# Kernel optimization log

Measured on AMD Instinct MI355X. Metric: run time of the kernel, lower is better.

The kernel has to match this reference:

```python
import jax, jax.numpy as jnp
import numpy as np

PARTS = [list(range(0, 17)), list(range(17, 22)), list(range(22, 27)),
         list(range(27, 36)), list(range(36, 42)), list(range(42, 48)),
         list(range(48, 68))]
NUM_PARTS = len(PARTS)
V_JOINTS = max(max(p) for p in PARTS) + 1  # 68
# joint -> part index (same as get_corr_joints)
JOINTS = np.zeros((V_JOINTS,), dtype=np.int32)
for j, part in enumerate(PARTS):
    for i in part:
        JOINTS[i] = j
BN_EPS = 1e-5


def setup_inputs() -> dict:
    key = jax.random.key(0)
    k0, k1, k2 = jax.random.split(key, 3)
    N, C, T, V = 512, 1024, 1, V_JOINTS
    x = jax.random.normal(k0, (N, C, T, V), dtype=jnp.float32)
    conv1_w = jax.random.normal(k1, (C // 4, C), dtype=jnp.float32) * 0.02  # 1x1 conv C->C/4
    conv1_b = jnp.zeros((C // 4,), dtype=jnp.float32)
    conv2_w = jax.random.normal(k2, (2,), dtype=jnp.float32) * 0.5  # 1x1 conv 2->1
    conv2_b = jnp.zeros((), dtype=jnp.float32)
    bn_gamma = jnp.ones((C,), dtype=jnp.float32)
    bn_beta = jnp.zeros((C,), dtype=jnp.float32)
    return {"x": x, "conv1_w": conv1_w, "conv1_b": conv1_b,
            "conv2_w": conv2_w, "conv2_b": conv2_b,
            "bn_gamma": bn_gamma, "bn_beta": bn_beta}


def _forward(x, conv1_w, conv1_b, conv2_w, conv2_b, bn_gamma, bn_beta):
    N, C, T, V = x.shape  # T must be 1 (required by original .view)
    joints = jnp.asarray(JOINTS)
    P = NUM_PARTS
    # part-wise mean pool over joints: (V,P) normalized one-hot
    M = jax.nn.one_hot(joints, P, dtype=x.dtype)
    M = M / jnp.sum(M, axis=0, keepdims=True)
    x_parts = jnp.einsum('nctv,vp->nctp', x, M)            # (N,C,T,P)
    # conv1: 1x1, C -> C/4
    h = jnp.einsum('nctp,oc->notp', x_parts, conv1_w) + conv1_b[None, :, None, None]
    x_cap = jnp.mean(h, axis=1, keepdims=True)             # channel avg pool
    x_cmp = jnp.max(h, axis=1, keepdims=True)              # channel max pool
    # conv2: 1x1, 2 -> 1 (cat order is (avg, max))
    att = conv2_w[0] * x_cap + conv2_w[1] * x_cmp + conv2_b  # (N,1,T,P)
    att = jnp.broadcast_to(att, (N, C, T, P)).reshape(N, C, P)
    att = jax.nn.softmax(att, axis=-1)                     # softmax over parts
    # scatter part attention back to joints
    att_j = att[:, :, joints][:, :, None, :]               # (N,C,1,V)
    y = x * att_j
    # BatchNorm2d (training mode: batch stats over N,T,V per channel)
    mean = jnp.mean(y, axis=(0, 2, 3), keepdims=True)
    var = jnp.var(y, axis=(0, 2, 3), keepdims=True)
    y_bn = (y - mean) * jax.lax.rsqrt(var + BN_EPS)
    y_bn = y_bn * bn_gamma[None, :, None, None] + bn_beta[None, :, None, None]
    return jax.nn.relu(y_bn + x)


def reference(x, conv1_w, conv1_b, conv2_w, conv2_b, bn_gamma, bn_beta):
    return _forward(x, conv1_w, conv1_b, conv2_w, conv2_b, bn_gamma, bn_beta)
```

## Files before the change

kernel.cpp:

```cpp
#include <hip/hip_runtime.h>

#define NN 512
#define CC 1024
#define OO 256
#define VV 68
#define PP 7
#define NC (NN*CC)
#define NV_CNT 34816.0f

__device__ __forceinline__ int part_of(int v){
  return (v>=17)+(v>=22)+(v>=27)+(v>=36)+(v>=42)+(v>=48);
}

__global__ __launch_bounds__(256) void k0_prep(const float* __restrict__ w1,
    float* __restrict__ w1p){
  int g = blockIdx.x*256 + threadIdx.x;
  int o = g >> 8, cb = g & 255;
  float4 v = ((const float4*)w1)[g];
  ((float4*)w1p)[cb*256 + o] = v;
}

__global__ __launch_bounds__(256) void k12_att(const float* __restrict__ x,
    const float* __restrict__ w1p, const float* __restrict__ b1,
    const float* __restrict__ w2, const float* __restrict__ b2,
    float* __restrict__ att, float* __restrict__ partial){
  int n = blockIdx.x;
  int t = threadIdx.x;

  __shared__ float stg[128*69];
  __shared__ float sS[PP*1024];
  __shared__ float red_s[4][PP], red_m[4][PP], pre[PP], att_s[PP];

  float q8[8][PP];
  #pragma unroll
  for (int cc=0;cc<8;cc++)
    #pragma unroll
    for (int p=0;p<PP;p++) q8[cc][p]=0.f;

  const float4* x4 = (const float4*)x;
  for (int cc=0; cc<8; cc++){
    int base = n*17408 + cc*2176;
    #pragma unroll
    for (int k=0;k<9;k++){
      int g = k*256 + t;
      if (k==8 && t>=128) break;
      float4 v = x4[base + g];
      int row = g/17, q = g - row*17;
      float* d = &stg[row*69 + q*4];
      d[0]=v.x; d[1]=v.y; d[2]=v.z; d[3]=v.w;
    }
    __syncthreads();
    if (t < 128){
      const float* r = &stg[t*69];
      int c = cc*128 + t;
      float s[PP];
      #pragma unroll
      for (int p=0;p<PP;p++) s[p]=0.f;
      #pragma unroll
      for (int v=0; v<VV; v++){
        int p = part_of(v);
        float e = r[v];
        s[p] += e;
        q8[cc][p] = fmaf(e, e, q8[cc][p]);
      }
      #pragma unroll
      for (int p=0;p<PP;p++) sS[p*1024 + c] = s[p];
    }
    __syncthreads();
  }

  int oh = t & 31, ch = t >> 5;
  float acc[8][PP];
  #pragma unroll
  for (int k=0;k<8;k++)
    #pragma unroll
    for (int p=0;p<PP;p++) acc[k][p] = 0.f;

  const float4* wp  = (const float4*)w1p;
  const float4* sf4 = (const float4*)sS;
  for (int i=0;i<32;i++){
    int gcb = ch*32 + i;
    const float4* wrow = wp + (size_t)gcb*256 + oh;
    float4 w[8];
    #pragma unroll
    for (int k=0;k<8;k++) w[k] = wrow[32*k];
    #pragma unroll
    for (int p=0;p<PP;p++){
      float4 sv = sf4[p*256 + gcb];
      #pragma unroll
      for (int k=0;k<8;k++){
        acc[k][p] = fmaf(w[k].x, sv.x, acc[k][p]);
        acc[k][p] = fmaf(w[k].y, sv.y, acc[k][p]);
        acc[k][p] = fmaf(w[k].z, sv.z, acc[k][p]);
        acc[k][p] = fmaf(w[k].w, sv.w, acc[k][p]);
      }
    }
  }

  const float inv_cnt[PP] = {1.f/17.f,1.f/5.f,1.f/5.f,1.f/9.f,1.f/6.f,1.f/6.f,1.f/20.f};
  float* hred = stg;
  float bo = b1[t];
  float h[PP];
  #pragma unroll
  for (int p=0;p<PP;p++){
    __syncthreads();
    #pragma unroll
    for (int k=0;k<8;k++) hred[ch*256 + k*32 + oh] = acc[k][p];
    __syncthreads();
    float hs = 0.f;
    #pragma unroll
    for (int c8=0;c8<8;c8++) hs += hred[c8*256 + t];
    h[p] = fmaf(hs, inv_cnt[p], bo);
  }

  int lane = t & 63, wid = t >> 6;
  #pragma unroll
  for (int p=0;p<PP;p++){
    float sm = h[p], mx = h[p];
    #pragma unroll
    for (int off=32; off>0; off>>=1){
      sm += __shfl_down(sm, off, 64);
      mx = fmaxf(mx, __shfl_down(mx, off, 64));
    }
    if (lane==0){ red_s[wid][p]=sm; red_m[wid][p]=mx; }
  }
  __syncthreads();
  if (t < PP){
    int p = t;
    float sm = red_s[0][p]+red_s[1][p]+red_s[2][p]+red_s[3][p];
    float mx = fmaxf(fmaxf(red_m[0][p],red_m[1][p]),
                     fmaxf(red_m[2][p],red_m[3][p]));
    pre[p] = w2[0]*(sm*(1.f/(float)OO)) + w2[1]*mx + b2[0];
  }
  __syncthreads();
  if (t == 0){
    float m = pre[0];
    #pragma unroll
    for (int p=1;p<PP;p++) m = fmaxf(m, pre[p]);
    float e[PP], sum=0.f;
    #pragma unroll
    for (int p=0;p<PP;p++){ e[p] = expf(pre[p]-m); sum += e[p]; }
    float inv = 1.f/sum;
    #pragma unroll
    for (int p=0;p<PP;p++){
      float a = e[p]*inv;
      att_s[p] = a;
      att[n*PP+p] = a;
    }
  }
  __syncthreads();

  if (t < 128){
    float a[PP], a2[PP];
    #pragma unroll
    for (int p=0;p<PP;p++){ a[p] = att_s[p]; a2[p] = a[p]*a[p]; }
    #pragma unroll
    for (int cc=0;cc<8;cc++){
      int c = cc*128 + t;
      float sm=0.f, sq=0.f;
      #pragma unroll
      for (int p=0;p<PP;p++){
        sm = fmaf(a[p],  sS[p*1024 + c], sm);
        sq = fmaf(a2[p], q8[cc][p],      sq);
      }
      partial[n*2048 + c]        = sm;
      partial[n*2048 + 1024 + c] = sq;
    }
  }
}

__global__ __launch_bounds__(256) void k3b1_reduce(const float* __restrict__ partial,
    float* __restrict__ p2){
  int nch = blockIdx.x >> 2, cb = blockIdx.x & 3;
  int c = cb*256 + threadIdx.x;
  float sm=0.f, sq=0.f;
  for (int i=0;i<64;i++){
    int n = nch*64 + i;
    sm += partial[n*2048 + c];
    sq += partial[n*2048 + 1024 + c];
  }
  p2[nch*2048 + c]        = sm;
  p2[nch*2048 + 1024 + c] = sq;
}

__global__ __launch_bounds__(256) void k3b2_finalize(const float* __restrict__ p2,
    const float* __restrict__ gamma, const float* __restrict__ beta,
    float* __restrict__ scsh){
  int c = blockIdx.x*256 + threadIdx.x;
  float sm=0.f, sq=0.f;
  #pragma unroll
  for (int ch=0;ch<8;ch++){
    sm += p2[ch*2048 + c];
    sq += p2[ch*2048 + 1024 + c];
  }
  float mean = sm * (1.0f/NV_CNT);
  float var  = sq * (1.0f/NV_CNT) - mean*mean;
  float rstd = rsqrtf(var + 1e-5f);
  float sc = gamma[c]*rstd;
  scsh[c]        = sc;
  scsh[1024 + c] = beta[c] - mean*sc;
}

__global__ __launch_bounds__(256) void k4_out(const float* __restrict__ x,
    const float* __restrict__ att, const float* __restrict__ scsh,
    float* __restrict__ out){
  int f = blockIdx.x*256 + threadIdx.x;
  int n = blockIdx.x / 68;
  __shared__ float s_att[PP];
  if (threadIdx.x < PP) s_att[threadIdx.x] = att[n*PP + threadIdx.x];
  __syncthreads();
  int r = f/17;
  int q = f - r*17;
  int v0 = q*4;
  int c = r & (CC-1);
  float4 xv = ((const float4*)x)[f];
  float sc = scsh[c];
  float sh = scsh[1024 + c];
  float vals[4];
  #pragma unroll
  for (int j=0;j<4;j++){
    int p = part_of(v0 + j);
    float a = s_att[p];
    float e = (j==0)?xv.x:(j==1)?xv.y:(j==2)?xv.z:xv.w;
    vals[j] = fmaxf(fmaf(e, fmaf(a, sc, 1.0f), sh), 0.0f);
  }
  float4 ov; ov.x=vals[0]; ov.y=vals[1]; ov.z=vals[2]; ov.w=vals[3];
  ((float4*)out)[f] = ov;
}

extern "C" void kernel_launch(void* const* d_in, const int* in_sizes, int n_in,
                              void* d_out, int out_size, void* d_ws, size_t ws_size,
                              hipStream_t stream) {
  const float* x     = (const float*)d_in[0];
  const float* w1    = (const float*)d_in[1];
  const float* b1    = (const float*)d_in[2];
  const float* w2    = (const float*)d_in[3];
  const float* b2    = (const float*)d_in[4];
  const float* gamma = (const float*)d_in[5];
  const float* beta  = (const float*)d_in[6];
  float* out = (float*)d_out;

  float* w1p     = (float*)d_ws;
  float* partial = w1p + OO*CC;
  float* p2      = partial + NN*2048;
  float* scsh    = p2 + 8*2048;
  float* att     = scsh + 2048;

  k0_prep      <<<256,         256, 0, stream>>>(w1, w1p);
  k12_att      <<<NN,          256, 0, stream>>>(x, w1p, b1, w2, b2, att, partial);
  k3b1_reduce  <<<32,          256, 0, stream>>>(partial, p2);
  k3b2_finalize<<<4,           256, 0, stream>>>(p2, gamma, beta, scsh);
  k4_out       <<<(NC*17)/256, 256, 0, stream>>>(x, att, scsh, out);
}
```

Before: 344.9 us.

## Split part-sum pass into its own wide kernel and fuse BN reduction stages

```diff
diff --git a/kernel.cpp b/kernel.cpp
--- a/kernel.cpp
+++ b/kernel.cpp
@@ -8,6 +8,8 @@
 #define NC (NN*CC)
 #define NV_CNT 34816.0f
 
+typedef float floatx4 __attribute__((ext_vector_type(4)));
+
 __device__ __forceinline__ int part_of(int v){
   return (v>=17)+(v>=22)+(v>=27)+(v>=36)+(v>=42)+(v>=48);
 }
@@ -20,54 +22,74 @@
   ((float4*)w1p)[cb*256 + o] = v;
 }
 
-__global__ __launch_bounds__(256) void k12_att(const float* __restrict__ x,
-    const float* __restrict__ w1p, const float* __restrict__ b1,
-    const float* __restrict__ w2, const float* __restrict__ b2,
-    float* __restrict__ att, float* __restrict__ partial){
+__global__ __launch_bounds__(256) void k1_partsum(const float* __restrict__ x,
+    float* __restrict__ S, float* __restrict__ S2){
+  __shared__ float stg[68*129];
+  int R = blockIdx.x*128;
+  const float4* src = (const float4*)(x + (size_t)R*VV);
+  #pragma unroll
+  for (int k=0;k<9;k++){
+    int g = k*256 + threadIdx.x;
+    if (k==8 && threadIdx.x>=128) break;
+    float4 v4 = src[g];
+    int row = g/17, q = g - row*17;
+    stg[(q*4+0)*129 + row] = v4.x;
+    stg[(q*4+1)*129 + row] = v4.y;
+    stg[(q*4+2)*129 + row] = v4.z;
+    stg[(q*4+3)*129 + row] = v4.w;
+  }
+  __syncthreads();
+
+  int row  = threadIdx.x & 127;
+  int half = threadIdx.x >> 7;
+  float s[PP], q2[PP];
+  #pragma unroll
+  for (int p=0;p<PP;p++){ s[p]=0.f; q2[p]=0.f; }
+  int v0 = half*34;
+  #pragma unroll
+  for (int i=0;i<34;i++){
+    int v = v0 + i;
+    int p = part_of(v);
+    float e = stg[v*129 + row];
+    s[p] += e;
+    q2[p] = fmaf(e, e, q2[p]);
+  }
+  __syncthreads();
+  float* hs = stg;
+  float* hq = stg + 128*PP;
+  if (half==1){
+    #pragma unroll
+    for (int p=0;p<PP;p++){ hs[row*PP+p]=s[p]; hq[row*PP+p]=q2[p]; }
+  }
+  __syncthreads();
+  if (half==0){
+    int r = R + row;
+    #pragma unroll
+    for (int p=0;p<PP;p++){
+      S [p*NC + r] = s[p]  + hs[row*PP+p];
+      S2[p*NC + r] = q2[p] + hq[row*PP+p];
+    }
+  }
+}
+
+__global__ __launch_bounds__(256) void k2_att(const float* __restrict__ S,
+    const float* __restrict__ S2, const float* __restrict__ w1p,
+    const float* __restrict__ b1, const float* __restrict__ w2,
+    const float* __restrict__ b2, float* __restrict__ att,
+    float* __restrict__ partial){
   int n = blockIdx.x;
   int t = threadIdx.x;
 
-  __shared__ float stg[128*69];
-  __shared__ float sS[PP*1024];
+  __shared__ float4 sSf4[PP*256];
+  __shared__ float hred[2048];
   __shared__ float red_s[4][PP], red_m[4][PP], pre[PP], att_s[PP];
-
-  float q8[8][PP];
-  #pragma unroll
-  for (int cc=0;cc<8;cc++)
-    #pragma unroll
-    for (int p=0;p<PP;p++) q8[cc][p]=0.f;
-
-  const float4* x4 = (const float4*)x;
-  for (int cc=0; cc<8; cc++){
-    int base = n*17408 + cc*2176;
-    #pragma unroll
-    for (int k=0;k<9;k++){
-      int g = k*256 + t;
-      if (k==8 && t>=128) break;
-      float4 v = x4[base + g];
-      int row = g/17, q = g - row*17;
-      float* d = &stg[row*69 + q*4];
-      d[0]=v.x; d[1]=v.y; d[2]=v.z; d[3]=v.w;
-    }
-    __syncthreads();
-    if (t < 128){
-      const float* r = &stg[t*69];
-      int c = cc*128 + t;
-      float s[PP];
-      #pragma unroll
-      for (int p=0;p<PP;p++) s[p]=0.f;
-      #pragma unroll
-      for (int v=0; v<VV; v++){
-        int p = part_of(v);
-        float e = r[v];
-        s[p] += e;
-        q8[cc][p] = fmaf(e, e, q8[cc][p]);
-      }
-      #pragma unroll
-      for (int p=0;p<PP;p++) sS[p*1024 + c] = s[p];
-    }
-    __syncthreads();
-  }
+  float* sSl = (float*)sSf4;
+
+  for (int u = t; u < PP*256; u += 256){
+    int p = u >> 8, cb = u & 255;
+    sSf4[u] = *(const float4*)(S + (size_t)p*NC + (size_t)n*CC + cb*4);
+  }
+  __syncthreads();
 
   int oh = t & 31, ch = t >> 5;
   float acc[8][PP];
@@ -76,8 +98,7 @@
     #pragma unroll
     for (int p=0;p<PP;p++) acc[k][p] = 0.f;
 
-  const float4* wp  = (const float4*)w1p;
-  const float4* sf4 = (const float4*)sS;
+  const float4* wp = (const float4*)w1p;
   for (int i=0;i<32;i++){
     int gcb = ch*32 + i;
     const float4* wrow = wp + (size_t)gcb*256 + oh;
@@ -86,7 +107,7 @@
     for (int k=0;k<8;k++) w[k] = wrow[32*k];
     #pragma unroll
     for (int p=0;p<PP;p++){
-      float4 sv = sf4[p*256 + gcb];
+      float4 sv = sSf4[p*256 + gcb];
       #pragma unroll
       for (int k=0;k<8;k++){
         acc[k][p] = fmaf(w[k].x, sv.x, acc[k][p]);
@@ -98,7 +119,6 @@
   }
 
   const float inv_cnt[PP] = {1.f/17.f,1.f/5.f,1.f/5.f,1.f/9.f,1.f/6.f,1.f/6.f,1.f/20.f};
-  float* hred = stg;
   float bo = b1[t];
   float h[PP];
   #pragma unroll
@@ -150,55 +170,50 @@
   }
   __syncthreads();
 
-  if (t < 128){
-    float a[PP], a2[PP];
-    #pragma unroll
-    for (int p=0;p<PP;p++){ a[p] = att_s[p]; a2[p] = a[p]*a[p]; }
-    #pragma unroll
-    for (int cc=0;cc<8;cc++){
-      int c = cc*128 + t;
-      float sm=0.f, sq=0.f;
-      #pragma unroll
-      for (int p=0;p<PP;p++){
-        sm = fmaf(a[p],  sS[p*1024 + c], sm);
-        sq = fmaf(a2[p], q8[cc][p],      sq);
-      }
-      partial[n*2048 + c]        = sm;
-      partial[n*2048 + 1024 + c] = sq;
-    }
-  }
-}
-
-__global__ __launch_bounds__(256) void k3b1_reduce(const float* __restrict__ partial,
-    float* __restrict__ p2){
-  int nch = blockIdx.x >> 2, cb = blockIdx.x & 3;
-  int c = cb*256 + threadIdx.x;
+  float a[PP], a2[PP];
+  #pragma unroll
+  for (int p=0;p<PP;p++){ a[p] = att_s[p]; a2[p] = a[p]*a[p]; }
+  const float* S2n = S2 + (size_t)n*CC;
+  #pragma unroll
+  for (int j=0;j<4;j++){
+    int c = j*256 + t;
+    float sm=0.f, sq=0.f;
+    #pragma unroll
+    for (int p=0;p<PP;p++){
+      sm = fmaf(a[p],  sSl[p*1024 + c],   sm);
+      sq = fmaf(a2[p], S2n[(size_t)p*NC + c], sq);
+    }
+    partial[n*2048 + c]        = sm;
+    partial[n*2048 + 1024 + c] = sq;
+  }
+}
+
+__global__ __launch_bounds__(256) void k3b_finalize(const float* __restrict__ partial,
+    const float* __restrict__ gamma, const float* __restrict__ beta,
+    float* __restrict__ scsh){
+  __shared__ float rs[8][32], rq[8][32];
+  int cl = threadIdx.x & 31, grp = threadIdx.x >> 5;
+  int c = blockIdx.x*32 + cl;
   float sm=0.f, sq=0.f;
   for (int i=0;i<64;i++){
-    int n = nch*64 + i;
+    int n = grp*64 + i;
     sm += partial[n*2048 + c];
     sq += partial[n*2048 + 1024 + c];
   }
-  p2[nch*2048 + c]        = sm;
-  p2[nch*2048 + 1024 + c] = sq;
-}
-
-__global__ __launch_bounds__(256) void k3b2_finalize(const float* __restrict__ p2,
-    const float* __restrict__ gamma, const float* __restrict__ beta,
-    float* __restrict__ scsh){
-  int c = blockIdx.x*256 + threadIdx.x;
-  float sm=0.f, sq=0.f;
-  #pragma unroll
-  for (int ch=0;ch<8;ch++){
-    sm += p2[ch*2048 + c];
-    sq += p2[ch*2048 + 1024 + c];
-  }
-  float mean = sm * (1.0f/NV_CNT);
-  float var  = sq * (1.0f/NV_CNT) - mean*mean;
-  float rstd = rsqrtf(var + 1e-5f);
-  float sc = gamma[c]*rstd;
-  scsh[c]        = sc;
-  scsh[1024 + c] = beta[c] - mean*sc;
+  rs[grp][cl] = sm; rq[grp][cl] = sq;
+  __syncthreads();
+  if (threadIdx.x < 32){
+    float tsm=0.f, tsq=0.f;
+    #pragma unroll
+    for (int g=0; g<8; g++){ tsm += rs[g][threadIdx.x]; tsq += rq[g][threadIdx.x]; }
+    int cc = blockIdx.x*32 + threadIdx.x;
+    float mean = tsm * (1.0f/NV_CNT);
+    float var  = tsq * (1.0f/NV_CNT) - mean*mean;
+    float rstd = rsqrtf(var + 1e-5f);
+    float sc = gamma[cc]*rstd;
+    scsh[cc]        = sc;
+    scsh[1024 + cc] = beta[cc] - mean*sc;
+  }
 }
 
 __global__ __launch_bounds__(256) void k4_out(const float* __restrict__ x,
@@ -224,8 +239,8 @@
     float e = (j==0)?xv.x:(j==1)?xv.y:(j==2)?xv.z:xv.w;
     vals[j] = fmaxf(fmaf(e, fmaf(a, sc, 1.0f), sh), 0.0f);
   }
-  float4 ov; ov.x=vals[0]; ov.y=vals[1]; ov.z=vals[2]; ov.w=vals[3];
-  ((float4*)out)[f] = ov;
+  floatx4 ov; ov.x=vals[0]; ov.y=vals[1]; ov.z=vals[2]; ov.w=vals[3];
+  __builtin_nontemporal_store(ov, ((floatx4*)out) + f);
 }
 
 extern "C" void kernel_launch(void* const* d_in, const int* in_sizes, int n_in,
@@ -241,14 +256,15 @@
   float* out = (float*)d_out;
 
   float* w1p     = (float*)d_ws;
-  float* partial = w1p + OO*CC;
-  float* p2      = partial + NN*2048;
-  float* scsh    = p2 + 8*2048;
+  float* S       = w1p + OO*CC;
+  float* S2      = S + 7*NC;
+  float* partial = S2 + 7*NC;
+  float* scsh    = partial + NN*2048;
   float* att     = scsh + 2048;
 
-  k0_prep      <<<256,         256, 0, stream>>>(w1, w1p);
-  k12_att      <<<NN,          256, 0, stream>>>(x, w1p, b1, w2, b2, att, partial);
-  k3b1_reduce  <<<32,          256, 0, stream>>>(partial, p2);
-  k3b2_finalize<<<4,           256, 0, stream>>>(p2, gamma, beta, scsh);
-  k4_out       <<<(NC*17)/256, 256, 0, stream>>>(x, att, scsh, out);
-}
+  k0_prep     <<<256,         256, 0, stream>>>(w1, w1p);
+  k1_partsum  <<<NC/128,      256, 0, stream>>>(x, S, S2);
+  k2_att      <<<NN,          256, 0, stream>>>(S, S2, w1p, b1, w2, b2, att, partial);
+  k3b_finalize<<<32,          256, 0, stream>>>(partial, gamma, beta, scsh);
+  k4_out      <<<(NC*17)/256, 256, 0, stream>>>(x, att, scsh, out);
+}
```

Measured after the change: 328.2 us. 4.8% less time.
